# Kernel optimization log

Measured on AMD Instinct MI355X. Metric: run time of the kernel, lower is better.

Reference implementation:

```python
import jax, jax.numpy as jnp
import numpy as np


def _apply_ry(state, c, s, wire):
    """Apply RY with cos/sin of theta/2 (c, s broadcastable over batch) on `wire`.
    PennyLane wire 0 is the most-significant qubit.
    state: [B, 2**Q] real float32."""
    B, N = state.shape
    st = state.reshape(B, 2 ** wire, 2, -1)
    a, b = st[:, :, 0], st[:, :, 1]
    st = jnp.stack([c * a - s * b, s * a + c * b], axis=2)
    return st.reshape(B, N)


def _apply_cnot_chain_step(state, ctrl):
    """CNOT with control=ctrl, target=ctrl+1 (adjacent wires)."""
    B, N = state.shape
    st = state.reshape(B, 2 ** ctrl, 2, 2, -1)
    st = jnp.stack([st[:, :, 0], st[:, :, 1, ::-1]], axis=2)
    return st.reshape(B, N)


def setup_inputs() -> dict:
    key = jax.random.key(0)
    k1, k2 = jax.random.split(key)
    B, Q, L = 512, 14, 2
    x = jax.random.normal(k1, (B, Q), dtype=jnp.float32)          # encoding angles
    weights = 0.5 * jax.random.normal(k2, (L, Q), dtype=jnp.float32)  # nn.Parameter randn*0.5
    return {"x": x, "weights": weights}


def reference(x, weights):
    B, Q = x.shape
    L = weights.shape[0]
    N_OUT = Q  # n_outputs == n_qubits here

    # |0...0> initial state, real-valued (RY and CNOT are real matrices)
    state = jnp.zeros((B, 2 ** Q), dtype=x.dtype).at[:, 0].set(1.0)

    # Angle encoding: RY(x_i) on wire i (per-sample angles)
    for i in range(Q):
        half = 0.5 * x[:, i]
        state = _apply_ry(state, jnp.cos(half)[:, None, None], jnp.sin(half)[:, None, None], i)

    # Variational layers: RY(weights[l, i]) per qubit, then CNOT ladder
    for l in range(L):
        for i in range(Q):
            half = 0.5 * weights[l, i]
            state = _apply_ry(state, jnp.cos(half), jnp.sin(half), i)
        for i in range(Q - 1):
            state = _apply_cnot_chain_step(state, i)

    # <Z_i> = P(wire i = 0) - P(wire i = 1)
    probs = state * state  # [B, 2**Q]
    outs = []
    for i in range(N_OUT):
        p = probs.reshape(B, 2 ** i, 2, -1).sum(axis=(1, 3))  # [B, 2]
        outs.append(p[:, 0] - p[:, 1])
    return jnp.stack(outs, axis=1).astype(jnp.float32)  # [B, n_outputs]
```

## Files before the change

kernel.cpp:

```cpp
#include <hip/hip_runtime.h>
#include <math.h>


#define Q 14
#define BLOCK 512
#define SCHUNK 36

template<int CTRL>
__device__ __forceinline__ float dppf(float v) {
    return __int_as_float(__builtin_amdgcn_update_dpp(
        0, __float_as_int(v), CTRL, 0xF, 0xF, true));
}
template<int OFF>
__device__ __forceinline__ float swzf(float v) {
    return __int_as_float(__builtin_amdgcn_ds_swizzle(__float_as_int(v), OFF));
}

__device__ __forceinline__ float sum32(float v) {
    v += dppf<0x121>(v);
    v += dppf<0x122>(v);
    v += dppf<0x124>(v);
    v += dppf<0x128>(v);
    v += swzf<0x401F>(v);
    return v;
}

template<int B2>
__device__ __forceinline__ void rpass2(float2 A[16], float c, float s) {
#pragma unroll
    for (int t = 0; t < 8; ++t) {
        const int j0 = ((t >> B2) << (B2 + 1)) | (t & ((1 << B2) - 1));
        const int j1 = j0 | (1 << B2);
        float2 a = A[j0], b = A[j1];
        A[j0] = make_float2(c * a.x - s * b.x, c * a.y - s * b.y);
        A[j1] = make_float2(s * a.x + c * b.x, s * a.y + c * b.y);
    }
}

__device__ __forceinline__ void rpass_intra(float2 A[16], float c, float s) {
#pragma unroll
    for (int j = 0; j < 16; ++j) {
        float2 a = A[j];
        A[j] = make_float2(c * a.x - s * a.y, s * a.x + c * a.y);
    }
}

__global__ __launch_bounds__(BLOCK, 4)
void quantum_kernel(const float* __restrict__ x,
                    const float* __restrict__ w,
                    float* __restrict__ out)
{
    alignas(16) __shared__ float lds[BLOCK * SCHUNK];
    __shared__ float2 cs0[Q], cs1[Q];
    __shared__ float red[16 * 12];

    const int b = blockIdx.x;
    const int tid = threadIdx.x;
    const int lane = tid & 63;

    if (tid < Q) {
        float a0 = 0.5f * (x[b * Q + tid] + w[tid]);
        cs0[tid] = make_float2(cosf(a0), sinf(a0));
        float a1 = 0.5f * w[Q + tid];
        cs1[tid] = make_float2(cosf(a1), sinf(a1));
    }
    __syncthreads();

    float H = 1.0f;
#pragma unroll
    for (int j = 0; j <= 7; ++j) {
        int gj = ((tid >> (j + 1)) ^ (tid >> j)) & 1;
        float2 f = cs0[13 - j];
        H *= gj ? f.y : f.x;
    }
    const int t8 = (tid >> 8) & 1;
    float2 f5 = cs0[5];
    float F5_0 = t8 ? f5.y : f5.x;
    float F5_1 = t8 ? f5.x : f5.y;
    float2 f4 = cs0[4], f3 = cs0[3], f2 = cs0[2], f1 = cs0[1], f0 = cs0[0];

    float2 A[16];
    {
        float t1[2], t2[4], t3[8], t4[16];
        t1[0] = H * F5_0;  t1[1] = H * F5_1;
#pragma unroll
        for (int r = 0; r < 4; ++r) {
            int g = ((r >> 1) ^ r) & 1;
            t2[r] = t1[r & 1] * (g ? f4.y : f4.x);
        }
#pragma unroll
        for (int r = 0; r < 8; ++r) {
            int g = ((r >> 2) ^ (r >> 1)) & 1;
            t3[r] = t2[r & 3] * (g ? f3.y : f3.x);
        }
#pragma unroll
        for (int r = 0; r < 16; ++r) {
            int g = ((r >> 3) ^ (r >> 2)) & 1;
            t4[r] = t3[r & 7] * (g ? f2.y : f2.x);
        }
        float FF00 = f0.x * f1.x;
        float FF01 = f0.x * f1.y;
        float FF10 = f0.y * f1.y;
        float FF11 = f0.y * f1.x;
#pragma unroll
        for (int j = 0; j < 16; ++j) {
            int r0 = 2 * j, r1 = 2 * j + 1;
            int a4 = (r0 >> 4) & 1, a3 = (r0 >> 3) & 1;
            int b4 = (r1 >> 4) & 1, b3 = (r1 >> 3) & 1;
            float Fa = a4 ? (a3 ? FF11 : FF10) : (a3 ? FF01 : FF00);
            float Fb = b4 ? (b3 ? FF11 : FF10) : (b3 ? FF01 : FF00);
            A[j] = make_float2(t4[r0 & 15] * Fa, t4[r1 & 15] * Fb);
        }
    }

    { float2 cs = cs1[0]; rpass2<3>(A, cs.x, cs.y); }
    { float2 cs = cs1[1]; rpass2<2>(A, cs.x, cs.y); }
    { float2 cs = cs1[2]; rpass2<1>(A, cs.x, cs.y); }
    { float2 cs = cs1[3]; rpass2<0>(A, cs.x, cs.y); }
    { float2 cs = cs1[4]; rpass_intra(A, cs.x, cs.y); }

    {
        const int base = (tid & 15) * SCHUNK + (tid >> 4);
#pragma unroll
        for (int j = 0; j < 16; ++j) {
            lds[base + ((2 * j) << 4) * SCHUNK]     = A[j].x;
            lds[base + ((2 * j + 1) << 4) * SCHUNK] = A[j].y;
        }
    }
    __syncthreads();
    {
        const float4* rp = (const float4*)&lds[tid * SCHUNK];
#pragma unroll
        for (int k = 0; k < 8; ++k) {
            float4 q = rp[k];
            A[2 * k]     = make_float2(q.x, q.y);
            A[2 * k + 1] = make_float2(q.z, q.w);
        }
    }

    { float2 cs = cs1[5]; rpass2<3>(A, cs.x, cs.y); }
    { float2 cs = cs1[6]; rpass2<2>(A, cs.x, cs.y); }
    { float2 cs = cs1[7]; rpass2<1>(A, cs.x, cs.y); }
    { float2 cs = cs1[8]; rpass2<0>(A, cs.x, cs.y); }
    { float2 cs = cs1[9]; rpass_intra(A, cs.x, cs.y); }

    {
        float2 cs = cs1[10];
        float sg = (lane & 8) ? cs.y : -cs.y;
#pragma unroll
        for (int j = 0; j < 16; ++j) {
            float px = dppf<0x128>(A[j].x);
            float py = dppf<0x128>(A[j].y);
            A[j] = make_float2(cs.x * A[j].x + sg * px,
                               cs.x * A[j].y + sg * py);
        }
    }
    {
        float2 cs = cs1[11];
        float sg = (lane & 4) ? cs.y : -cs.y;
#pragma unroll
        for (int j = 0; j < 16; ++j) {
            float px = swzf<0x101F>(A[j].x);
            float py = swzf<0x101F>(A[j].y);
            A[j] = make_float2(cs.x * A[j].x + sg * px,
                               cs.x * A[j].y + sg * py);
        }
    }
    {
        float2 cs = cs1[12];
        float sg = (lane & 2) ? cs.y : -cs.y;
#pragma unroll
        for (int j = 0; j < 16; ++j) {
            float px = dppf<0x4E>(A[j].x);
            float py = dppf<0x4E>(A[j].y);
            A[j] = make_float2(cs.x * A[j].x + sg * px,
                               cs.x * A[j].y + sg * py);
        }
    }
    {
        float2 cs = cs1[13];
        float sg = (lane & 1) ? cs.y : -cs.y;
#pragma unroll
        for (int j = 0; j < 16; ++j) {
            float px = dppf<0xB1>(A[j].x);
            float py = dppf<0xB1>(A[j].y);
            A[j] = make_float2(cs.x * A[j].x + sg * px,
                               cs.x * A[j].y + sg * py);
        }
    }

    float2 acV0 = make_float2(0.f, 0.f), acV1 = acV0, acV2 = acV0,
           acV3 = acV0, acV4 = acV0, acV5 = acV0;
#pragma unroll
    for (int j = 0; j < 16; ++j) {
        float2 v = A[j];
        float2 p = make_float2(v.x * v.x, v.y * v.y);
        acV0 = make_float2(acV0.x + p.x, acV0.y + p.y);
        const float s1 = ((j >> 3) & 1) ? -1.f : 1.f;
        const float s2 = (__builtin_popcount(j >> 2) & 1) ? -1.f : 1.f;
        const float s3 = (__builtin_popcount(j >> 1) & 1) ? -1.f : 1.f;
        const float s4 = (__builtin_popcount(j) & 1) ? -1.f : 1.f;
        acV1 = make_float2(acV1.x + s1 * p.x, acV1.y + s1 * p.y);
        acV2 = make_float2(acV2.x + s2 * p.x, acV2.y + s2 * p.y);
        acV3 = make_float2(acV3.x + s3 * p.x, acV3.y + s3 * p.y);
        acV4 = make_float2(acV4.x + s4 * p.x, acV4.y + s4 * p.y);
        acV5 = make_float2(acV5.x + s4 * p.x, acV5.y - s4 * p.y);
    }
    float acc0 = acV0.x + acV0.y;
    float acc1 = acV1.x + acV1.y;
    float acc2 = acV2.x + acV2.y;
    float acc3 = acV3.x + acV3.y;
    float acc4 = acV4.x + acV4.y;
    float acc5 = acV5.x + acV5.y;

    const int ll = lane & 31;
    const float g4 = ((ll >> 4) & 1) ? -1.f : 1.f;
    const float g3 = (__builtin_popcount(ll >> 3) & 1) ? -1.f : 1.f;
    const float g2 = (__builtin_popcount(ll >> 2) & 1) ? -1.f : 1.f;
    const float g1 = (__builtin_popcount(ll >> 1) & 1) ? -1.f : 1.f;
    const float g0 = (__builtin_popcount(ll) & 1) ? -1.f : 1.f;

    float R0  = sum32(acc0);
    float R1  = sum32(g4 * acc0);
    float R2  = sum32(g4 * acc1);
    float R3  = sum32(g4 * acc2);
    float R4  = sum32(g4 * acc3);
    float R5  = sum32(g4 * acc4);
    float R6  = sum32(g4 * acc5);
    float R7  = sum32(g3 * acc5);
    float R8  = sum32(g2 * acc5);
    float R9  = sum32(g1 * acc5);
    float R10 = sum32(g0 * acc5);

    if (ll == 0) {
        float* rp = &red[(tid >> 5) * 12];
        rp[0] = R0;  rp[1] = R1;  rp[2] = R2;  rp[3] = R3;
        rp[4] = R4;  rp[5] = R5;  rp[6] = R6;  rp[7] = R7;
        rp[8] = R8;  rp[9] = R9;  rp[10] = R10;
    }
    __syncthreads();

    if (tid < Q) {
        const int k = (tid <= 3) ? 0 : (tid - 3);
        const int sh = (tid == 0) ? 3 : (tid == 1) ? 2 : (tid == 2) ? 1 : 0;
        float s = 0.f;
#pragma unroll
        for (int h = 0; h < 16; ++h) {
            float r = red[h * 12 + k];
            s += (__builtin_popcount(h >> sh) & 1) ? -r : r;
        }
        out[b * Q + tid] = s;
    }
}

extern "C" void kernel_launch(void* const* d_in, const int* in_sizes, int n_in,
                              void* d_out, int out_size, void* d_ws, size_t ws_size,
                              hipStream_t stream) {
    const float* x = (const float*)d_in[0];
    const float* w = (const float*)d_in[1];
    float* out = (float*)d_out;
    const int B = in_sizes[0] / Q;
    quantum_kernel<<<dim3(B), dim3(BLOCK), 0, stream>>>(x, w, out);
}
```

Measured before the change: 63.33 us.

## Replace full statevector simulation with closed-form per-sample expectation recurrence

Drops the 16K-amplitude statevector simulation (one 512-thread block per sample, LDS transpose, cross-lane shuffles and reductions) in favour of an analytic recurrence. It tracks a small 2x2 reduced quantity along the CNOT chain, with one thread per batch sample. The aim is to remove nearly all arithmetic and synchronisation, since the fixed circuit structure (product-state encoding, one weight layer folded in, CNOT ladder) gives a closed form. The risk is that correctness depends on the derivation matching this exact circuit, with L=2 layers and this particular gate ordering.

```diff
diff --git a/kernel.cpp b/kernel.cpp
--- a/kernel.cpp
+++ b/kernel.cpp
@@ -3,253 +3,42 @@
 
 
 #define Q 14
-#define BLOCK 512
-#define SCHUNK 36
 
-template<int CTRL>
-__device__ __forceinline__ float dppf(float v) {
-    return __int_as_float(__builtin_amdgcn_update_dpp(
-        0, __float_as_int(v), CTRL, 0xF, 0xF, true));
-}
-template<int OFF>
-__device__ __forceinline__ float swzf(float v) {
-    return __int_as_float(__builtin_amdgcn_ds_swizzle(__float_as_int(v), OFF));
-}
-
-__device__ __forceinline__ float sum32(float v) {
-    v += dppf<0x121>(v);
-    v += dppf<0x122>(v);
-    v += dppf<0x124>(v);
-    v += dppf<0x128>(v);
-    v += swzf<0x401F>(v);
-    return v;
-}
-
-template<int B2>
-__device__ __forceinline__ void rpass2(float2 A[16], float c, float s) {
-#pragma unroll
-    for (int t = 0; t < 8; ++t) {
-        const int j0 = ((t >> B2) << (B2 + 1)) | (t & ((1 << B2) - 1));
-        const int j1 = j0 | (1 << B2);
-        float2 a = A[j0], b = A[j1];
-        A[j0] = make_float2(c * a.x - s * b.x, c * a.y - s * b.y);
-        A[j1] = make_float2(s * a.x + c * b.x, s * a.y + c * b.y);
-    }
-}
-
-__device__ __forceinline__ void rpass_intra(float2 A[16], float c, float s) {
-#pragma unroll
-    for (int j = 0; j < 16; ++j) {
-        float2 a = A[j];
-        A[j] = make_float2(c * a.x - s * a.y, s * a.x + c * a.y);
-    }
-}
-
-__global__ __launch_bounds__(BLOCK, 4)
+__global__ __launch_bounds__(64)
 void quantum_kernel(const float* __restrict__ x,
                     const float* __restrict__ w,
-                    float* __restrict__ out)
+                    float* __restrict__ out,
+                    int B)
 {
-    alignas(16) __shared__ float lds[BLOCK * SCHUNK];
-    __shared__ float2 cs0[Q], cs1[Q];
-    __shared__ float red[16 * 12];
+    const int b = blockIdx.x * 64 + threadIdx.x;
+    if (b >= B) return;
 
-    const int b = blockIdx.x;
-    const int tid = threadIdx.x;
-    const int lane = tid & 63;
-
-    if (tid < Q) {
-        float a0 = 0.5f * (x[b * Q + tid] + w[tid]);
-        cs0[tid] = make_float2(cosf(a0), sinf(a0));
-        float a1 = 0.5f * w[Q + tid];
-        cs1[tid] = make_float2(cosf(a1), sinf(a1));
-    }
-    __syncthreads();
-
-    float H = 1.0f;
+    float ca[Q], sa[Q], s2a[Q], cw[Q], sw[Q];
 #pragma unroll
-    for (int j = 0; j <= 7; ++j) {
-        int gj = ((tid >> (j + 1)) ^ (tid >> j)) & 1;
-        float2 f = cs0[13 - j];
-        H *= gj ? f.y : f.x;
-    }
-    const int t8 = (tid >> 8) & 1;
-    float2 f5 = cs0[5];
-    float F5_0 = t8 ? f5.y : f5.x;
-    float F5_1 = t8 ? f5.x : f5.y;
-    float2 f4 = cs0[4], f3 = cs0[3], f2 = cs0[2], f1 = cs0[1], f0 = cs0[0];
-
-    float2 A[16];
-    {
-        float t1[2], t2[4], t3[8], t4[16];
-        t1[0] = H * F5_0;  t1[1] = H * F5_1;
-#pragma unroll
-        for (int r = 0; r < 4; ++r) {
-            int g = ((r >> 1) ^ r) & 1;
-            t2[r] = t1[r & 1] * (g ? f4.y : f4.x);
-        }
-#pragma unroll
-        for (int r = 0; r < 8; ++r) {
-            int g = ((r >> 2) ^ (r >> 1)) & 1;
-            t3[r] = t2[r & 3] * (g ? f3.y : f3.x);
-        }
-#pragma unroll
-        for (int r = 0; r < 16; ++r) {
-            int g = ((r >> 3) ^ (r >> 2)) & 1;
-            t4[r] = t3[r & 7] * (g ? f2.y : f2.x);
-        }
-        float FF00 = f0.x * f1.x;
-        float FF01 = f0.x * f1.y;
-        float FF10 = f0.y * f1.y;
-        float FF11 = f0.y * f1.x;
-#pragma unroll
-        for (int j = 0; j < 16; ++j) {
-            int r0 = 2 * j, r1 = 2 * j + 1;
-            int a4 = (r0 >> 4) & 1, a3 = (r0 >> 3) & 1;
-            int b4 = (r1 >> 4) & 1, b3 = (r1 >> 3) & 1;
-            float Fa = a4 ? (a3 ? FF11 : FF10) : (a3 ? FF01 : FF00);
-            float Fb = b4 ? (b3 ? FF11 : FF10) : (b3 ? FF01 : FF00);
-            A[j] = make_float2(t4[r0 & 15] * Fa, t4[r1 & 15] * Fb);
-        }
+    for (int j = 0; j < Q; ++j) {
+        float alpha = 0.5f * (x[b * Q + j] + w[j]);
+        float s, c;
+        sincosf(alpha, &s, &c);
+        ca[j] = c;
+        sa[j] = s;
+        s2a[j] = 2.0f * c * s;
+        sincosf(w[Q + j], &sw[j], &cw[j]);
     }
 
-    { float2 cs = cs1[0]; rpass2<3>(A, cs.x, cs.y); }
-    { float2 cs = cs1[1]; rpass2<2>(A, cs.x, cs.y); }
-    { float2 cs = cs1[2]; rpass2<1>(A, cs.x, cs.y); }
-    { float2 cs = cs1[3]; rpass2<0>(A, cs.x, cs.y); }
-    { float2 cs = cs1[4]; rpass_intra(A, cs.x, cs.y); }
-
-    {
-        const int base = (tid & 15) * SCHUNK + (tid >> 4);
+    float f00 = 1.0f, f11 = 0.0f, f01 = 0.0f;
 #pragma unroll
-        for (int j = 0; j < 16; ++j) {
-            lds[base + ((2 * j) << 4) * SCHUNK]     = A[j].x;
-            lds[base + ((2 * j + 1) << 4) * SCHUNK] = A[j].y;
-        }
-    }
-    __syncthreads();
-    {
-        const float4* rp = (const float4*)&lds[tid * SCHUNK];
-#pragma unroll
-        for (int k = 0; k < 8; ++k) {
-            float4 q = rp[k];
-            A[2 * k]     = make_float2(q.x, q.y);
-            A[2 * k + 1] = make_float2(q.z, q.w);
-        }
-    }
-
-    { float2 cs = cs1[5]; rpass2<3>(A, cs.x, cs.y); }
-    { float2 cs = cs1[6]; rpass2<2>(A, cs.x, cs.y); }
-    { float2 cs = cs1[7]; rpass2<1>(A, cs.x, cs.y); }
-    { float2 cs = cs1[8]; rpass2<0>(A, cs.x, cs.y); }
-    { float2 cs = cs1[9]; rpass_intra(A, cs.x, cs.y); }
-
-    {
-        float2 cs = cs1[10];
-        float sg = (lane & 8) ? cs.y : -cs.y;
-#pragma unroll
-        for (int j = 0; j < 16; ++j) {
-            float px = dppf<0x128>(A[j].x);
-            float py = dppf<0x128>(A[j].y);
-            A[j] = make_float2(cs.x * A[j].x + sg * px,
-                               cs.x * A[j].y + sg * py);
-        }
-    }
-    {
-        float2 cs = cs1[11];
-        float sg = (lane & 4) ? cs.y : -cs.y;
-#pragma unroll
-        for (int j = 0; j < 16; ++j) {
-            float px = swzf<0x101F>(A[j].x);
-            float py = swzf<0x101F>(A[j].y);
-            A[j] = make_float2(cs.x * A[j].x + sg * px,
-                               cs.x * A[j].y + sg * py);
-        }
-    }
-    {
-        float2 cs = cs1[12];
-        float sg = (lane & 2) ? cs.y : -cs.y;
-#pragma unroll
-        for (int j = 0; j < 16; ++j) {
-            float px = dppf<0x4E>(A[j].x);
-            float py = dppf<0x4E>(A[j].y);
-            A[j] = make_float2(cs.x * A[j].x + sg * px,
-                               cs.x * A[j].y + sg * py);
-        }
-    }
-    {
-        float2 cs = cs1[13];
-        float sg = (lane & 1) ? cs.y : -cs.y;
-#pragma unroll
-        for (int j = 0; j < 16; ++j) {
-            float px = dppf<0xB1>(A[j].x);
-            float py = dppf<0xB1>(A[j].y);
-            A[j] = make_float2(cs.x * A[j].x + sg * px,
-                               cs.x * A[j].y + sg * py);
-        }
-    }
-
-    float2 acV0 = make_float2(0.f, 0.f), acV1 = acV0, acV2 = acV0,
-           acV3 = acV0, acV4 = acV0, acV5 = acV0;
-#pragma unroll
-    for (int j = 0; j < 16; ++j) {
-        float2 v = A[j];
-        float2 p = make_float2(v.x * v.x, v.y * v.y);
-        acV0 = make_float2(acV0.x + p.x, acV0.y + p.y);
-        const float s1 = ((j >> 3) & 1) ? -1.f : 1.f;
-        const float s2 = (__builtin_popcount(j >> 2) & 1) ? -1.f : 1.f;
-        const float s3 = (__builtin_popcount(j >> 1) & 1) ? -1.f : 1.f;
-        const float s4 = (__builtin_popcount(j) & 1) ? -1.f : 1.f;
-        acV1 = make_float2(acV1.x + s1 * p.x, acV1.y + s1 * p.y);
-        acV2 = make_float2(acV2.x + s2 * p.x, acV2.y + s2 * p.y);
-        acV3 = make_float2(acV3.x + s3 * p.x, acV3.y + s3 * p.y);
-        acV4 = make_float2(acV4.x + s4 * p.x, acV4.y + s4 * p.y);
-        acV5 = make_float2(acV5.x + s4 * p.x, acV5.y - s4 * p.y);
-    }
-    float acc0 = acV0.x + acV0.y;
-    float acc1 = acV1.x + acV1.y;
-    float acc2 = acV2.x + acV2.y;
-    float acc3 = acV3.x + acV3.y;
-    float acc4 = acV4.x + acV4.y;
-    float acc5 = acV5.x + acV5.y;
-
-    const int ll = lane & 31;
-    const float g4 = ((ll >> 4) & 1) ? -1.f : 1.f;
-    const float g3 = (__builtin_popcount(ll >> 3) & 1) ? -1.f : 1.f;
-    const float g2 = (__builtin_popcount(ll >> 2) & 1) ? -1.f : 1.f;
-    const float g1 = (__builtin_popcount(ll >> 1) & 1) ? -1.f : 1.f;
-    const float g0 = (__builtin_popcount(ll) & 1) ? -1.f : 1.f;
-
-    float R0  = sum32(acc0);
-    float R1  = sum32(g4 * acc0);
-    float R2  = sum32(g4 * acc1);
-    float R3  = sum32(g4 * acc2);
-    float R4  = sum32(g4 * acc3);
-    float R5  = sum32(g4 * acc4);
-    float R6  = sum32(g4 * acc5);
-    float R7  = sum32(g3 * acc5);
-    float R8  = sum32(g2 * acc5);
-    float R9  = sum32(g1 * acc5);
-    float R10 = sum32(g0 * acc5);
-
-    if (ll == 0) {
-        float* rp = &red[(tid >> 5) * 12];
-        rp[0] = R0;  rp[1] = R1;  rp[2] = R2;  rp[3] = R3;
-        rp[4] = R4;  rp[5] = R5;  rp[6] = R6;  rp[7] = R7;
-        rp[8] = R8;  rp[9] = R9;  rp[10] = R10;
-    }
-    __syncthreads();
-
-    if (tid < Q) {
-        const int k = (tid <= 3) ? 0 : (tid - 3);
-        const int sh = (tid == 0) ? 3 : (tid == 1) ? 2 : (tid == 2) ? 1 : 0;
-        float s = 0.f;
-#pragma unroll
-        for (int h = 0; h < 16; ++h) {
-            float r = red[h * 12 + k];
-            s += (__builtin_popcount(h >> sh) & 1) ? -r : r;
-        }
-        out[b * Q + tid] = s;
+    for (int j = 0; j < Q; ++j) {
+        const float c = ca[j], s = sa[j];
+        const float cc = c * c, ss = s * s, cs = c * s;
+        const float cross = 2.0f * cs * f01;
+        const float h00 = cc * f00 + cross + ss * f11;
+        const float h11 = ss * f00 + cross + cc * f11;
+        const float h01 = cs * (f00 + f11) + f01;
+        f00 = cw[j] * h00;
+        f11 = -cw[j] * h11;
+        f01 = -sw[j] * h01;
+        const float g = (j < Q - 1) ? s2a[j + 1] : 1.0f;
+        out[b * Q + j] = f00 + f11 + 2.0f * g * f01;
     }
 }
 
@@ -260,5 +49,6 @@
     const float* w = (const float*)d_in[1];
     float* out = (float*)d_out;
     const int B = in_sizes[0] / Q;
-    quantum_kernel<<<dim3(B), dim3(BLOCK), 0, stream>>>(x, w, out);
+    const int grid = (B + 63) / 64;
+    quantum_kernel<<<dim3(grid), dim3(64), 0, stream>>>(x, w, out, B);
 }
```

Result: faster. 57.85 us (-8.7%).
